# Performance work log

Hardware: AMD Instinct MI355X
Metric: run time of the kernel (lower is better)

The kernel has to match this reference:

```python
import jax, jax.numpy as jnp
import numpy as np

B, T, LQ, LC = 8, 256, 20, 10
DIM, H = 128, 8
VDIM, WDIM, CDIM = 1024, 300, 50
WORDS, CHARS = 10000, 100


def _build_edges(T, B):
    """Replicates build_graph_edges(hops=2) + build_semantic_edges + build_query_edges,
    then expand_edge_index_for_batch with num_nodes = T + 1.  Static numpy (jit-safe)."""
    N = T + 1
    es = []
    for h in (1, 2):  # temporal edges, 2 hops (indices replicate original code exactly)
        i = np.arange(T - h)
        es += [np.stack([i, i + h]), np.stack([i + h, i])]
    i = np.arange(T)  # query<->segment edges inside build_graph_edges
    z = np.zeros(T, dtype=np.int64)
    es += [np.stack([z, i + 1]), np.stack([i + 1, z])]
    temporal = np.concatenate(es, axis=1)
    a, b = np.triu_indices(T, k=1)  # torch.combinations(arange(T), r=2)
    sem = np.concatenate([np.stack([a, b]), np.stack([b, a])], axis=1)
    qe = np.stack([np.concatenate([[0], np.arange(1, T + 1)]),
                   np.concatenate([np.arange(1, T + 1), [0]])])
    off = (np.arange(B, dtype=np.int64) * N)[None, :, None]
    expand = lambda e: (e[:, None, :].astype(np.int64) + off).reshape(2, -1)
    return np.concatenate([expand(temporal), expand(sem), expand(qe)], axis=1)


def setup_inputs() -> dict:
    key = jax.random.key(0)
    ks = jax.random.split(key, 16)
    w = lambda k, shape: jax.random.normal(k, shape, jnp.float32) * 0.02
    return {
        "word_ids": jax.random.randint(ks[0], (B, LQ), 0, WORDS),
        "char_ids": jax.random.randint(ks[1], (B, LQ, LC), 0, CHARS),
        "video_features": jax.random.normal(ks[2], (B, T, VDIM), jnp.float32),
        "v_mask": jnp.ones((B, T), jnp.float32),
        "q_mask": jnp.ones((B, LQ), jnp.float32),
        "word_emb": w(ks[3], (WORDS, WDIM)),
        "char_emb": w(ks[4], (CHARS, CDIM)),
        "W_embed": w(ks[5], (WDIM + CDIM, DIM)), "b_embed": jnp.zeros((DIM,), jnp.float32),
        "W_vproj": w(ks[6], (VDIM, DIM)), "b_vproj": jnp.zeros((DIM,), jnp.float32),
        "W_enc": w(ks[7], (DIM, DIM)), "b_enc": jnp.zeros((DIM,), jnp.float32),
        "Wq": w(ks[8], (DIM, DIM)), "bq": jnp.zeros((DIM,), jnp.float32),
        "Wk": w(ks[9], (DIM, DIM)), "bk": jnp.zeros((DIM,), jnp.float32),
        "Wv": w(ks[10], (DIM, DIM)), "bv": jnp.zeros((DIM,), jnp.float32),
        "Wskip": w(ks[11], (DIM, DIM)), "bskip": jnp.zeros((DIM,), jnp.float32),
        "W_start": w(ks[12], (DIM, 1)), "b_start": jnp.zeros((1,), jnp.float32),
        "W_end": w(ks[13], (DIM, 1)), "b_end": jnp.zeros((1,), jnp.float32),
    }


def reference(word_ids, char_ids, video_features, v_mask, q_mask,
              word_emb, char_emb, W_embed, b_embed, W_vproj, b_vproj,
              W_enc, b_enc, Wq, bq, Wk, bk, Wv, bv, Wskip, bskip,
              W_start, b_start, W_end, b_end):
    enc = lambda x, m: jax.nn.relu(x @ W_enc + b_enc) * m[..., None]  # shared feature encoder (stand-in)
    # video branch
    vfeat = enc(video_features @ W_vproj + b_vproj, v_mask)            # [B, T, DIM]
    # query branch: word + char embeddings -> dim, encode, mean-pool
    qemb = jnp.concatenate([word_emb[word_ids], char_emb[char_ids].mean(axis=2)], axis=-1)
    qfeat = enc(qemb @ W_embed + b_embed, q_mask).mean(axis=1)         # [B, DIM]
    nodes = jnp.concatenate([qfeat[:, None, :], vfeat], axis=1)        # [B, N, DIM], N = T+1
    Bn, N, _ = nodes.shape
    Nn = Bn * N
    xf = nodes.reshape(Nn, DIM)
    edges = jnp.asarray(_build_edges(N - 1, Bn))                       # [2, E] static
    src, dst = edges[0], edges[1]                                      # PyG: messages x_j=src -> target i=dst
    hd = DIM // H
    q = (xf @ Wq + bq).reshape(Nn, H, hd)
    k = (xf @ Wk + bk).reshape(Nn, H, hd)
    v = (xf @ Wv + bv).reshape(Nn, H, hd)
    # TransformerConv: per-edge attention logits, segment-softmax over incoming edges
    logits = (q[dst] * k[src]).sum(-1) / float(np.sqrt(hd))            # [E, H]
    mx = jax.ops.segment_max(logits, dst, num_segments=Nn)
    ex = jnp.exp(logits - mx[dst])
    den = jax.ops.segment_sum(ex, dst, num_segments=Nn)
    alpha = ex / (den[dst] + 1e-16)
    agg = jax.ops.segment_sum(alpha[:, :, None] * v[src], dst, num_segments=Nn)  # [Nn, H, hd]
    out = agg.reshape(Nn, DIM) + xf @ Wskip + bskip                    # root_weight skip connection
    out = out.reshape(Bn, N, DIM)
    start_logits = (out[:, 1:] @ W_start + b_start)[..., 0]            # [B, T]
    end_logits = (out[:, 1:] @ W_end + b_end)[..., 0]                  # [B, T]
    return start_logits, end_logits
```

## Files before the change

### kernel.cpp

```cpp
#include <hip/hip_runtime.h>
#include <hip/hip_bf16.h>
#include <math.h>

#define B_ 8
#define T_ 256
#define LQ_ 20
#define LC_ 10
#define DIM_ 128
#define N_ 257
#define NN_ (B_*N_)

#define FMA4(a, s, ww) { (a).x += (s)*(ww).x; (a).y += (s)*(ww).y; (a).z += (s)*(ww).z; (a).w += (s)*(ww).w; }

__global__ __launch_bounds__(512) void kNODE(
    const float* __restrict__ video, const float* __restrict__ Wv,
    const float* __restrict__ bvp,
    const float* __restrict__ We, const float* __restrict__ be,
    const float* __restrict__ vmask,
    const int* __restrict__ word_ids, const int* __restrict__ char_ids,
    const float* __restrict__ word_emb, const float* __restrict__ char_emb,
    const float* __restrict__ W_embed, const float* __restrict__ b_embed,
    const float* __restrict__ q_mask,
    const float* __restrict__ Wq, const float* __restrict__ bq,
    const float* __restrict__ Wk, const float* __restrict__ bk,
    const float* __restrict__ Wvv, const float* __restrict__ bval,
    const float* __restrict__ Ws, const float* __restrict__ bs,
    float* __restrict__ q, float* __restrict__ k,
    float* __restrict__ v, float* __restrict__ sk,
    float* __restrict__ eq)
{
  __shared__ __align__(16) float smem_f[9504];
  float4* ps4 = reinterpret_cast<float4*>(smem_f);
  float* hl = smem_f + 8448;
  float* xe = smem_f + 8976;
  const int blk = blockIdx.x, tid = threadIdx.x;
  const float* Wm[4] = {Wq, Wk, Wvv, Ws};
  const float* bm[4] = {bq, bk, bval, bs};
  float* om[4] = {q, k, v, sk};

  if (blk < 512) {
    const int r0 = blk * 4;
    const int c4 = tid & 31, ks = tid >> 5;
    float4 acc[4];
    #pragma unroll
    for (int r = 0; r < 4; ++r) acc[r] = float4{0.f, 0.f, 0.f, 0.f};
    {
      const float4* W4 = reinterpret_cast<const float4*>(Wv) + c4;
      const float* vbase = video + (size_t)r0 * 1024;
      for (int kc = 0; kc < 16; ++kc) {
        const int k0 = ks * 64 + kc * 4;
        const float4 w0 = W4[(size_t)(k0 + 0) * 32];
        const float4 w1 = W4[(size_t)(k0 + 1) * 32];
        const float4 w2 = W4[(size_t)(k0 + 2) * 32];
        const float4 w3 = W4[(size_t)(k0 + 3) * 32];
        const float4 x0 = *reinterpret_cast<const float4*>(vbase + 0 * 1024 + k0);
        const float4 x1 = *reinterpret_cast<const float4*>(vbase + 1 * 1024 + k0);
        const float4 x2 = *reinterpret_cast<const float4*>(vbase + 2 * 1024 + k0);
        const float4 x3 = *reinterpret_cast<const float4*>(vbase + 3 * 1024 + k0);
        FMA4(acc[0], x0.x, w0); FMA4(acc[0], x0.y, w1); FMA4(acc[0], x0.z, w2); FMA4(acc[0], x0.w, w3);
        FMA4(acc[1], x1.x, w0); FMA4(acc[1], x1.y, w1); FMA4(acc[1], x1.z, w2); FMA4(acc[1], x1.w, w3);
        FMA4(acc[2], x2.x, w0); FMA4(acc[2], x2.y, w1); FMA4(acc[2], x2.z, w2); FMA4(acc[2], x2.w, w3);
        FMA4(acc[3], x3.x, w0); FMA4(acc[3], x3.y, w1); FMA4(acc[3], x3.z, w2); FMA4(acc[3], x3.w, w3);
      }
    }
    #pragma unroll
    for (int r = 0; r < 4; ++r) ps4[(ks * 4 + r) * 33 + c4] = acc[r];
    __syncthreads();
    if (tid < 128) {
      const int r = tid >> 5, c = tid & 31;
      float4 s = reinterpret_cast<const float4*>(bvp)[c];
      #pragma unroll
      for (int ke = 0; ke < 16; ++ke) {
        const float4 p = ps4[(ke * 4 + r) * 33 + c];
        s.x += p.x; s.y += p.y; s.z += p.z; s.w += p.w;
      }
      *reinterpret_cast<float4*>(&hl[r * 132 + c * 4]) = s;
    }
    __syncthreads();
    #pragma unroll
    for (int r = 0; r < 4; ++r) acc[r] = float4{0.f, 0.f, 0.f, 0.f};
    {
      const float4* We4 = reinterpret_cast<const float4*>(We) + c4;
      #pragma unroll
      for (int kc = 0; kc < 2; ++kc) {
        const int k0 = ks * 8 + kc * 4;
        const float4 w0 = We4[(size_t)(k0 + 0) * 32];
        const float4 w1 = We4[(size_t)(k0 + 1) * 32];
        const float4 w2 = We4[(size_t)(k0 + 2) * 32];
        const float4 w3 = We4[(size_t)(k0 + 3) * 32];
        #pragma unroll
        for (int r = 0; r < 4; ++r) {
          const float4 rv = *reinterpret_cast<const float4*>(&hl[r * 132 + k0]);
          FMA4(acc[r], rv.x, w0); FMA4(acc[r], rv.y, w1);
          FMA4(acc[r], rv.z, w2); FMA4(acc[r], rv.w, w3);
        }
      }
    }
    __syncthreads();
    #pragma unroll
    for (int r = 0; r < 4; ++r) ps4[(ks * 4 + r) * 33 + c4] = acc[r];
    __syncthreads();
    if (tid < 128) {
      const int r = tid >> 5, c = tid & 31;
      float4 s = reinterpret_cast<const float4*>(be)[c];
      #pragma unroll
      for (int ke = 0; ke < 16; ++ke) {
        const float4 p = ps4[(ke * 4 + r) * 33 + c];
        s.x += p.x; s.y += p.y; s.z += p.z; s.w += p.w;
      }
      const float mk = vmask[r0 + r];
      s.x = fmaxf(s.x, 0.f) * mk; s.y = fmaxf(s.y, 0.f) * mk;
      s.z = fmaxf(s.z, 0.f) * mk; s.w = fmaxf(s.w, 0.f) * mk;
      *reinterpret_cast<float4*>(&xe[r * 132 + c * 4]) = s;
    }
    __syncthreads();
    const int m = ks >> 2, keP = ks & 3;
    #pragma unroll
    for (int r = 0; r < 4; ++r) acc[r] = float4{0.f, 0.f, 0.f, 0.f};
    {
      const float4* Wp4 = reinterpret_cast<const float4*>(Wm[m]) + c4;
      #pragma unroll
      for (int kc = 0; kc < 8; ++kc) {
        const int k0 = keP * 32 + kc * 4;
        const float4 w0 = Wp4[(size_t)(k0 + 0) * 32];
        const float4 w1 = Wp4[(size_t)(k0 + 1) * 32];
        const float4 w2 = Wp4[(size_t)(k0 + 2) * 32];
        const float4 w3 = Wp4[(size_t)(k0 + 3) * 32];
        #pragma unroll
        for (int r = 0; r < 4; ++r) {
          const float4 rv = *reinterpret_cast<const float4*>(&xe[r * 132 + k0]);
          FMA4(acc[r], rv.x, w0); FMA4(acc[r], rv.y, w1);
          FMA4(acc[r], rv.z, w2); FMA4(acc[r], rv.w, w3);
        }
      }
    }
    __syncthreads();
    #pragma unroll
    for (int r = 0; r < 4; ++r) ps4[(ks * 4 + r) * 33 + c4] = acc[r];
    __syncthreads();
    {
      const int mm = tid >> 7, r = (tid >> 5) & 3, c = tid & 31;
      float4 s = reinterpret_cast<const float4*>(bm[mm])[c];
      #pragma unroll
      for (int ke = 0; ke < 4; ++ke) {
        const float4 p = ps4[((mm * 4 + ke) * 4 + r) * 33 + c];
        s.x += p.x; s.y += p.y; s.z += p.z; s.w += p.w;
      }
      const int vr = r0 + r;
      const int node = (vr >> 8) * 257 + 1 + (vr & 255);
      *reinterpret_cast<float4*>(om[mm] + (size_t)node * 128 + 4 * c) = s;
    }
  } else {
    const int qi = blk - 512;
    const int b = qi / 20, lq = qi - b * 20;
    float* emb = smem_f;
    float* ps  = emb + 352;
    float* hq  = emb + 608;
    float* pe  = emb + 736;
    const int wid = word_ids[b * LQ_ + lq];
    for (int m2 = tid; m2 < 300; m2 += 512) emb[m2] = word_emb[(size_t)wid * 300 + m2];
    if (tid < 50) {
      float s = 0.f;
      #pragma unroll
      for (int l = 0; l < 10; ++l) {
        const int cid = char_ids[(b * LQ_ + lq) * 10 + l];
        s += char_emb[cid * 50 + tid];
      }
      emb[300 + tid] = s * 0.1f;
    }
    __syncthreads();
    const int j = tid & 127, half = tid >> 7;
    if (tid < 256) {
      float a = 0.f;
      const float* Wcol = W_embed + (size_t)(half * 175) * 128 + j;
      const float* eh = emb + half * 175;
      #pragma unroll 5
      for (int m2 = 0; m2 < 175; ++m2) a += eh[m2] * Wcol[(size_t)m2 * 128];
      ps[half * 128 + j] = a;
    }
    __syncthreads();
    if (tid < 128) hq[tid] = ps[tid] + ps[128 + tid] + b_embed[tid];
    __syncthreads();
    if (tid < 256) {
      float e = 0.f;
      #pragma unroll 8
      for (int kk = 0; kk < 64; ++kk)
        e += hq[half * 64 + kk] * We[(half * 64 + kk) * 128 + j];
      pe[half * 128 + j] = e;
    }
    __syncthreads();
    if (tid < 128) {
      float ev = pe[tid] + pe[128 + tid] + be[tid];
      ev = fmaxf(ev, 0.f) * q_mask[b * LQ_ + lq];
      eq[(size_t)qi * 128 + tid] = ev;
    }
  }
}

__device__ __forceinline__ float cntf(int dnode, int s) {
  if (dnode == 256) return (s == 0 ? 1.f : 0.f) + (s == 255 ? 1.f : 0.f);
  float c = (s != dnode) ? 1.f : 0.f;
  if (s == 0) c += 1.f;
  if (s == dnode - 1) c += 2.f;
  if (s == dnode + 1 && dnode <= 254) c += 1.f;
  if (s == dnode - 2 && dnode >= 2) c += 1.f;
  if (s == dnode + 2 && dnode <= 253) c += 1.f;
  return c;
}

__global__ __launch_bounds__(256) void kATTN(
    const float* __restrict__ q, const float* __restrict__ k,
    const float* __restrict__ v, const float* __restrict__ eq,
    const float* __restrict__ Wk, const float* __restrict__ bk,
    const float* __restrict__ Wvv, const float* __restrict__ bval,
    float* __restrict__ npart, float* __restrict__ dpart)
{
  __shared__ float Kl[32][128];
  __shared__ float Vl[32][128];
  __shared__ float m0[128];
  const int d0 = blockIdx.x * 32;
  const int y  = blockIdx.y;
  const int b  = blockIdx.z;
  const int tid = threadIdx.x;
  const int base = b * 257;
  const int s0 = y * 32;
  {
    const float4* ksrc = reinterpret_cast<const float4*>(k + (size_t)(base + s0) * 128);
    const float4* vsrc = reinterpret_cast<const float4*>(v + (size_t)(base + s0) * 128);
    float4* kd = reinterpret_cast<float4*>(Kl);
    float4* vd = reinterpret_cast<float4*>(Vl);
    #pragma unroll
    for (int i = 0; i < 4; ++i) {
      kd[tid + i * 256] = ksrc[tid + i * 256];
      vd[tid + i * 256] = vsrc[tid + i * 256];
    }
  }
  if (y == 0 && tid < 128) {
    float s = 0.f;
    #pragma unroll 4
    for (int lq = 0; lq < LQ_; ++lq) s += eq[((size_t)b * LQ_ + lq) * 128 + tid];
    m0[tid] = s * (1.f / LQ_);
  }
  const int dd = tid >> 3, h = tid & 7;
  const int dnode = d0 + dd + 1;
  const float* qrow = q + (size_t)(base + dnode) * 128 + h * 16;
  const float4 qq0 = *(const float4*)(qrow + 0);
  const float4 qq1 = *(const float4*)(qrow + 4);
  const float4 qq2 = *(const float4*)(qrow + 8);
  const float4 qq3 = *(const float4*)(qrow + 12);
  __syncthreads();
  if (y == 0) {
    const int j = tid & 127, half = tid >> 7;
    const float* W = half ? Wvv : Wk;
    float acc = half ? bval[j] : bk[j];
    #pragma unroll 8
    for (int kk = 0; kk < 128; ++kk) acc += m0[kk] * W[kk * 128 + j];
    if (half) Vl[0][j] = acc; else Kl[0][j] = acc;
  }
  __syncthreads();

  float den = 0.f;
  float4 o0 = {0,0,0,0}, o1 = {0,0,0,0}, o2 = {0,0,0,0}, o3 = {0,0,0,0};
  #pragma unroll 2
  for (int s = 0; s < 32; ++s) {
    const float* krow = &Kl[s][h * 16];
    const float4 k0 = *(const float4*)(krow + 0);
    const float4 k1 = *(const float4*)(krow + 4);
    const float4 k2 = *(const float4*)(krow + 8);
    const float4 k3 = *(const float4*)(krow + 12);
    float dt = qq0.x*k0.x + qq0.y*k0.y + qq0.z*k0.z + qq0.w*k0.w
             + qq1.x*k1.x + qq1.y*k1.y + qq1.z*k1.z + qq1.w*k1.w
             + qq2.x*k2.x + qq2.y*k2.y + qq2.z*k2.z + qq2.w*k2.w
             + qq3.x*k3.x + qq3.y*k3.y + qq3.z*k3.z + qq3.w*k3.w;
    const float c = cntf(dnode, s0 + s);
    const float pw = c * __expf(dt * 0.25f);
    den += pw;
    const float* vrow = &Vl[s][h * 16];
    const float4 v0 = *(const float4*)(vrow + 0);
    const float4 v1 = *(const float4*)(vrow + 4);
    const float4 v2 = *(const float4*)(vrow + 8);
    const float4 v3 = *(const float4*)(vrow + 12);
    o0.x += pw*v0.x; o0.y += pw*v0.y; o0.z += pw*v0.z; o0.w += pw*v0.w;
    o1.x += pw*v1.x; o1.y += pw*v1.y; o1.z += pw*v1.z; o1.w += pw*v1.w;
    o2.x += pw*v2.x; o2.y += pw*v2.y; o2.z += pw*v2.z; o2.w += pw*v2.w;
    o3.x += pw*v3.x; o3.y += pw*v3.y; o3.z += pw*v3.z; o3.w += pw*v3.w;
  }
  const size_t pb = ((size_t)y * 8 + b) * 256 + d0;
  float* np = npart + (pb + dd) * 128 + h * 16;
  *reinterpret_cast<float4*>(np + 0)  = o0;
  *reinterpret_cast<float4*>(np + 4)  = o1;
  *reinterpret_cast<float4*>(np + 8)  = o2;
  *reinterpret_cast<float4*>(np + 12) = o3;
  dpart[(pb + dd) * 8 + h] = den;
}

__global__ __launch_bounds__(256) void kRED(
    const float* __restrict__ npart, const float* __restrict__ dpart,
    const float* __restrict__ sk,
    const float* __restrict__ W_start, const float* __restrict__ b_start,
    const float* __restrict__ W_end, const float* __restrict__ b_end,
    float* __restrict__ out)
{
  __shared__ float red[16][2][2];
  const int d0 = blockIdx.x * 16;
  const int b = blockIdx.y;
  const int tid = threadIdx.x;
  const int base = b * 257;
  const int jB = tid & 127, shB = tid >> 7;
  const int hB = jB >> 4;
  const float wst = W_start[jB], wen = W_end[jB];
  #pragma unroll
  for (int dd8 = 0; dd8 < 8; ++dd8) {
    const int dd = shB * 8 + dd8;
    const int dst = d0 + dd;
    float num = 0.f, den = 0.f;
    #pragma unroll
    for (int y = 0; y < 8; ++y) {
      const size_t pb = ((size_t)y * 8 + b) * 256 + dst;
      num += npart[pb * 128 + jB];
      den += dpart[pb * 8 + hB];
    }
    const float o = num / (den + 1e-16f) + sk[(size_t)(base + dst + 1) * 128 + jB];
    float psum = o * wst, pesum = o * wen;
    #pragma unroll
    for (int off = 1; off < 64; off <<= 1) {
      psum += __shfl_xor(psum, off);
      pesum += __shfl_xor(pesum, off);
    }
    if ((tid & 63) == 0) { red[dd][jB >> 6][0] = psum; red[dd][jB >> 6][1] = pesum; }
  }
  __syncthreads();
  if (tid < 16) {
    out[b * 256 + d0 + tid]        = red[tid][0][0] + red[tid][1][0] + b_start[0];
    out[2048 + b * 256 + d0 + tid] = red[tid][0][1] + red[tid][1][1] + b_end[0];
  }
}

extern "C" void kernel_launch(void* const* d_in, const int* in_sizes, int n_in,
                              void* d_out, int out_size, void* d_ws, size_t ws_size,
                              hipStream_t stream) {
  const int*   word_ids = (const int*)d_in[0];
  const int*   char_ids = (const int*)d_in[1];
  const float* video    = (const float*)d_in[2];
  const float* v_mask   = (const float*)d_in[3];
  const float* q_mask   = (const float*)d_in[4];
  const float* word_emb = (const float*)d_in[5];
  const float* char_emb = (const float*)d_in[6];
  const float* W_embed  = (const float*)d_in[7];
  const float* b_embed  = (const float*)d_in[8];
  const float* W_vproj  = (const float*)d_in[9];
  const float* b_vproj  = (const float*)d_in[10];
  const float* W_enc    = (const float*)d_in[11];
  const float* b_enc    = (const float*)d_in[12];
  const float* Wq       = (const float*)d_in[13];
  const float* bq       = (const float*)d_in[14];
  const float* Wk       = (const float*)d_in[15];
  const float* bk       = (const float*)d_in[16];
  const float* Wv       = (const float*)d_in[17];
  const float* bv       = (const float*)d_in[18];
  const float* Wskip    = (const float*)d_in[19];
  const float* bskip    = (const float*)d_in[20];
  const float* W_start  = (const float*)d_in[21];
  const float* b_start  = (const float*)d_in[22];
  const float* W_end    = (const float*)d_in[23];
  const float* b_end    = (const float*)d_in[24];

  float* q     = (float*)d_ws;
  float* k     = q  + NN_ * DIM_;
  float* v     = k  + NN_ * DIM_;
  float* sk    = v  + NN_ * DIM_;
  float* eq    = sk + NN_ * DIM_;
  float* npart = eq + 160 * 128;
  float* dpart = npart + (size_t)8 * 8 * 256 * 128;

  hipLaunchKernelGGL(kNODE, dim3(672), dim3(512), 0, stream,
    video, W_vproj, b_vproj, W_enc, b_enc, v_mask,
    word_ids, char_ids, word_emb, char_emb, W_embed, b_embed, q_mask,
    Wq, bq, Wk, bk, Wv, bv, Wskip, bskip, q, k, v, sk, eq);
  hipLaunchKernelGGL(kATTN, dim3(8, 8, 8), dim3(256), 0, stream,
    q, k, v, eq, Wk, bk, Wv, bv, npart, dpart);
  hipLaunchKernelGGL(kRED, dim3(16, 8), dim3(256), 0, stream,
    npart, dpart, sk, W_start, b_start, W_end, b_end, (float*)d_out);
}
```

Before: 61.35 us.

## Stage video rows in LDS and pre-reduce split-K partials with wave shuffles

Each block now loads its four 1024-wide video rows cooperatively into shared memory once, instead of every thread fetching them from global memory directly. The split-K partial sums in all three GEMM stages are first combined across the two 32-lane halves of each 64-wide wavefront with xor-32 shuffles, so only half the threads write partials to LDS and the final reductions read half as many entries. This shrinks shared memory from about 38KB to about 21KB, which may allow more blocks per CU. It adds an extra barrier and LDS reads in the inner loop in place of broadcast global loads.

```diff
diff --git a/kernel.cpp b/kernel.cpp
--- a/kernel.cpp
+++ b/kernel.cpp
@@ -11,6 +11,8 @@
 #define NN_ (B_*N_)
 
 #define FMA4(a, s, ww) { (a).x += (s)*(ww).x; (a).y += (s)*(ww).y; (a).z += (s)*(ww).z; (a).w += (s)*(ww).w; }
+#define PAIR4(a) { (a).x += __shfl_xor((a).x, 32); (a).y += __shfl_xor((a).y, 32); \
+                   (a).z += __shfl_xor((a).z, 32); (a).w += __shfl_xor((a).w, 32); }
 
 __global__ __launch_bounds__(512) void kNODE(
     const float* __restrict__ video, const float* __restrict__ Wv,
@@ -29,10 +31,10 @@
     float* __restrict__ v, float* __restrict__ sk,
     float* __restrict__ eq)
 {
-  __shared__ __align__(16) float smem_f[9504];
+  __shared__ __align__(16) float smem_f[5280];
   float4* ps4 = reinterpret_cast<float4*>(smem_f);
-  float* hl = smem_f + 8448;
-  float* xe = smem_f + 8976;
+  float* hl = smem_f + 4224;
+  float* xe = smem_f + 4752;
   const int blk = blockIdx.x, tid = threadIdx.x;
   const float* Wm[4] = {Wq, Wk, Wvv, Ws};
   const float* bm[4] = {bq, bk, bval, bs};
@@ -40,38 +42,51 @@
 
   if (blk < 512) {
     const int r0 = blk * 4;
+    {
+      const float4* src = reinterpret_cast<const float4*>(video + (size_t)r0 * 1024);
+      #pragma unroll
+      for (int i = 0; i < 2; ++i) {
+        const int idx4 = tid + i * 512;
+        const int r = idx4 >> 8, f = idx4 & 255;
+        *reinterpret_cast<float4*>(&smem_f[r * 1028 + f * 4]) = src[r * 256 + f];
+      }
+    }
+    __syncthreads();
     const int c4 = tid & 31, ks = tid >> 5;
+    const int lane32 = ((tid & 63) < 32);
     float4 acc[4];
     #pragma unroll
     for (int r = 0; r < 4; ++r) acc[r] = float4{0.f, 0.f, 0.f, 0.f};
     {
       const float4* W4 = reinterpret_cast<const float4*>(Wv) + c4;
-      const float* vbase = video + (size_t)r0 * 1024;
       for (int kc = 0; kc < 16; ++kc) {
         const int k0 = ks * 64 + kc * 4;
         const float4 w0 = W4[(size_t)(k0 + 0) * 32];
         const float4 w1 = W4[(size_t)(k0 + 1) * 32];
         const float4 w2 = W4[(size_t)(k0 + 2) * 32];
         const float4 w3 = W4[(size_t)(k0 + 3) * 32];
-        const float4 x0 = *reinterpret_cast<const float4*>(vbase + 0 * 1024 + k0);
-        const float4 x1 = *reinterpret_cast<const float4*>(vbase + 1 * 1024 + k0);
-        const float4 x2 = *reinterpret_cast<const float4*>(vbase + 2 * 1024 + k0);
-        const float4 x3 = *reinterpret_cast<const float4*>(vbase + 3 * 1024 + k0);
-        FMA4(acc[0], x0.x, w0); FMA4(acc[0], x0.y, w1); FMA4(acc[0], x0.z, w2); FMA4(acc[0], x0.w, w3);
-        FMA4(acc[1], x1.x, w0); FMA4(acc[1], x1.y, w1); FMA4(acc[1], x1.z, w2); FMA4(acc[1], x1.w, w3);
-        FMA4(acc[2], x2.x, w0); FMA4(acc[2], x2.y, w1); FMA4(acc[2], x2.z, w2); FMA4(acc[2], x2.w, w3);
-        FMA4(acc[3], x3.x, w0); FMA4(acc[3], x3.y, w1); FMA4(acc[3], x3.z, w2); FMA4(acc[3], x3.w, w3);
-      }
-    }
-    #pragma unroll
-    for (int r = 0; r < 4; ++r) ps4[(ks * 4 + r) * 33 + c4] = acc[r];
+        #pragma unroll
+        for (int r = 0; r < 4; ++r) {
+          const float4 rv = *reinterpret_cast<const float4*>(&smem_f[r * 1028 + k0]);
+          FMA4(acc[r], rv.x, w0); FMA4(acc[r], rv.y, w1);
+          FMA4(acc[r], rv.z, w2); FMA4(acc[r], rv.w, w3);
+        }
+      }
+    }
+    #pragma unroll
+    for (int r = 0; r < 4; ++r) PAIR4(acc[r]);
+    __syncthreads();
+    if (lane32) {
+      #pragma unroll
+      for (int r = 0; r < 4; ++r) ps4[((ks >> 1) * 4 + r) * 33 + c4] = acc[r];
+    }
     __syncthreads();
     if (tid < 128) {
       const int r = tid >> 5, c = tid & 31;
       float4 s = reinterpret_cast<const float4*>(bvp)[c];
       #pragma unroll
-      for (int ke = 0; ke < 16; ++ke) {
-        const float4 p = ps4[(ke * 4 + r) * 33 + c];
+      for (int g = 0; g < 8; ++g) {
+        const float4 p = ps4[(g * 4 + r) * 33 + c];
         s.x += p.x; s.y += p.y; s.z += p.z; s.w += p.w;
       }
       *reinterpret_cast<float4*>(&hl[r * 132 + c * 4]) = s;
@@ -96,16 +111,20 @@
         }
       }
     }
-    __syncthreads();
-    #pragma unroll
-    for (int r = 0; r < 4; ++r) ps4[(ks * 4 + r) * 33 + c4] = acc[r];
+    #pragma unroll
+    for (int r = 0; r < 4; ++r) PAIR4(acc[r]);
+    __syncthreads();
+    if (lane32) {
+      #pragma unroll
+      for (int r = 0; r < 4; ++r) ps4[((ks >> 1) * 4 + r) * 33 + c4] = acc[r];
+    }
     __syncthreads();
     if (tid < 128) {
       const int r = tid >> 5, c = tid & 31;
       float4 s = reinterpret_cast<const float4*>(be)[c];
       #pragma unroll
-      for (int ke = 0; ke < 16; ++ke) {
-        const float4 p = ps4[(ke * 4 + r) * 33 + c];
+      for (int g = 0; g < 8; ++g) {
+        const float4 p = ps4[(g * 4 + r) * 33 + c];
         s.x += p.x; s.y += p.y; s.z += p.z; s.w += p.w;
       }
       const float mk = vmask[r0 + r];
@@ -114,14 +133,14 @@
       *reinterpret_cast<float4*>(&xe[r * 132 + c * 4]) = s;
     }
     __syncthreads();
-    const int m = ks >> 2, keP = ks & 3;
+    const int m = ks >> 2, ks4 = ks & 3;
     #pragma unroll
     for (int r = 0; r < 4; ++r) acc[r] = float4{0.f, 0.f, 0.f, 0.f};
     {
       const float4* Wp4 = reinterpret_cast<const float4*>(Wm[m]) + c4;
       #pragma unroll
       for (int kc = 0; kc < 8; ++kc) {
-        const int k0 = keP * 32 + kc * 4;
+        const int k0 = ks4 * 32 + kc * 4;
         const float4 w0 = Wp4[(size_t)(k0 + 0) * 32];
         const float4 w1 = Wp4[(size_t)(k0 + 1) * 32];
         const float4 w2 = Wp4[(size_t)(k0 + 2) * 32];
@@ -134,18 +153,21 @@
         }
       }
     }
-    __syncthreads();
-    #pragma unroll
-    for (int r = 0; r < 4; ++r) ps4[(ks * 4 + r) * 33 + c4] = acc[r];
+    #pragma unroll
+    for (int r = 0; r < 4; ++r) PAIR4(acc[r]);
+    __syncthreads();
+    if (lane32) {
+      #pragma unroll
+      for (int r = 0; r < 4; ++r) ps4[((m * 2 + (ks4 >> 1)) * 4 + r) * 33 + c4] = acc[r];
+    }
     __syncthreads();
     {
       const int mm = tid >> 7, r = (tid >> 5) & 3, c = tid & 31;
       float4 s = reinterpret_cast<const float4*>(bm[mm])[c];
-      #pragma unroll
-      for (int ke = 0; ke < 4; ++ke) {
-        const float4 p = ps4[((mm * 4 + ke) * 4 + r) * 33 + c];
-        s.x += p.x; s.y += p.y; s.z += p.z; s.w += p.w;
-      }
+      const float4 p0 = ps4[((mm * 2 + 0) * 4 + r) * 33 + c];
+      const float4 p1 = ps4[((mm * 2 + 1) * 4 + r) * 33 + c];
+      s.x += p0.x + p1.x; s.y += p0.y + p1.y;
+      s.z += p0.z + p1.z; s.w += p0.w + p1.w;
       const int vr = r0 + r;
       const int node = (vr >> 8) * 257 + 1 + (vr & 255);
       *reinterpret_cast<float4*>(om[mm] + (size_t)node * 128 + 4 * c) = s;
```

New measurement: 62.08 us. About the same (+1.2%).
